# Kernel optimization log

Measured on AMD Instinct MI355X. Metric: run time of the kernel, lower is better.

Reference implementation:

```python
import jax, jax.numpy as jnp
import numpy as np

V = 128            # target_size (blank = V-1)
H = 2              # context_history_size
EMB = 128          # context_embedding_dim
ENC = 512          # enc_dim
PRED = 256         # pred_dim
JOIN = 512         # joiner_dim
B, T, U = 8, 512, 64


def setup_inputs() -> dict:
    key = jax.random.key(0)
    ks = jax.random.split(key, 12)
    s = lambda *d: 1.0 / np.sqrt(d[0])
    emb = jax.random.normal(ks[0], (V, EMB), jnp.float32) * 0.02
    emb = emb.at[V - 1].set(0.0)  # padding_idx row is zero
    inp = {
        "encoder_states": jax.random.normal(ks[1], (B, T, ENC), jnp.float32),
        "encoder_states_size": jnp.maximum(jax.random.randint(ks[2], (B,), 0, T + 1), 1).astype(jnp.int32),
        "targets": jax.random.randint(ks[3], (B, U), 0, V - 1, jnp.int64),
        "targets_size": jnp.maximum(jax.random.randint(ks[4], (B,), 0, U + 1), 1).astype(jnp.int32),
        "emb": emb,
        "W1": jax.random.normal(ks[5], (H * EMB, PRED), jnp.float32) * s(H * EMB),
        "b1": jnp.zeros((PRED,), jnp.float32),
        "W2": jax.random.normal(ks[6], (PRED, PRED), jnp.float32) * s(PRED),
        "b2": jnp.zeros((PRED,), jnp.float32),
        "Wj1": jax.random.normal(ks[7], (ENC + PRED, JOIN), jnp.float32) * s(ENC + PRED),
        "bj1": jnp.zeros((JOIN,), jnp.float32),
        "Wj2": jax.random.normal(ks[8], (JOIN, V), jnp.float32) * s(JOIN),
        "bj2": jnp.zeros((V,), jnp.float32),
    }
    return inp


def reference(encoder_states, encoder_states_size, targets, targets_size,
              emb, W1, b1, W2, b2, Wj1, bj1, Wj2, bj2):
    # ---- prediction network ----
    ext = jnp.pad(targets, ((0, 0), (H, 0)), constant_values=V - 1)  # [B, U+H]
    L = ext.shape[1]
    # context[..., i] = ext[:, H-1-i : L-i]  -> shape [B, U+1, H]
    context = jnp.stack([ext[:, H - 1 - i: L - i] for i in range(H)], axis=-1)
    e = emb[context].reshape(targets.shape[0], U + 1, H * EMB)  # [B, U+1, H*EMB]
    p = jax.nn.relu(e @ W1 + b1)
    pred = jax.nn.relu(p @ W2 + b2)                              # [B, U+1, PRED]

    # ---- joint network (dense masked T x (U+1) grid; concat-linear split into two GEMMs) ----
    We, Wp = Wj1[:ENC], Wj1[ENC:]
    enc_proj = jnp.einsum('bte,ej->btj', encoder_states, We)     # [B, T, JOIN]
    pred_proj = jnp.einsum('bup,pj->buj', pred, Wp)              # [B, U+1, JOIN]
    h = jax.nn.relu(enc_proj[:, :, None, :] + pred_proj[:, None, :, :] + bj1)  # [B,T,U+1,JOIN]
    logits = h @ Wj2 + bj2                                       # [B, T, U+1, V]

    t_idx = jnp.arange(T)[None, :, None]
    u_idx = jnp.arange(U + 1)[None, None, :]
    mask = (t_idx < encoder_states_size[:, None, None]) & (u_idx <= targets_size[:, None, None])
    return logits * mask[..., None].astype(logits.dtype)
```

## Files before the change

### kernel.cpp

```cpp
#include <hip/hip_runtime.h>


#define VOCAB 128
#define EMBD  128
#define ENCD  512
#define PREDD 256
#define JOIND 512
#define NB    8
#define NT    512
#define NUT   64
#define UP1   65
#define PRROWS 4

typedef __fp16   pk16x2 __attribute__((ext_vector_type(2)));
typedef _Float16 f16x8  __attribute__((ext_vector_type(8)));
typedef float    f32x4  __attribute__((ext_vector_type(4)));

__device__ __forceinline__ float frelu(float x) { return x > 0.f ? x : 0.f; }

__device__ __forceinline__ void splitf16_2(float x0, float x1,
                                           unsigned& hi, unsigned& lo) {
    pk16x2 h = __builtin_amdgcn_cvt_pkrtz(x0, x1);
    float r0 = x0 - (float)h.x;
    float r1 = x1 - (float)h.y;
    pk16x2 l = __builtin_amdgcn_cvt_pkrtz(r0, r1);
    __builtin_memcpy(&hi, &h, 4);
    __builtin_memcpy(&lo, &l, 4);
}

__global__ __launch_bounds__(256) void prep_weights(
    const float* __restrict__ Wj2, const float* __restrict__ Wj1,
    unsigned short* __restrict__ WjF, unsigned short* __restrict__ WeF)
{
    const int idx = blockIdx.x * 256 + threadIdx.x;
    float x; unsigned short* dst;
    if (idx < VOCAB * JOIND) {
        const int c = idx >> 12, rem = idx & 4095;
        const int n = rem >> 5, p = (rem >> 3) & 3, e = rem & 7;
        const int k = c * 32 + ((p ^ (n & 3)) << 3) + e;
        x = Wj2[k * VOCAB + n];
        dst = WjF + idx;
    } else {
        const int j = idx - VOCAB * JOIND;
        const int ct = j >> 16, rem1 = j & 65535;
        const int c = rem1 >> 12, rem = rem1 & 4095;
        const int nl = rem >> 5, p = (rem >> 3) & 3, e = rem & 7;
        const int n = ct * 128 + nl;
        const int k = c * 32 + ((p ^ (nl & 3)) << 3) + e;
        x = Wj1[(size_t)k * JOIND + n];
        dst = WeF + j;
    }
    const _Float16 h = (_Float16)x;
    unsigned short bits; __builtin_memcpy(&bits, &h, 2);
    *dst = bits;
}

__global__ __launch_bounds__(256, 3) void fused_pe(
    const int* __restrict__ targets, const int* __restrict__ tsz,
    const float* __restrict__ emb,
    const float* __restrict__ W1, const float* __restrict__ b1,
    const float* __restrict__ W2, const float* __restrict__ b2,
    const float* __restrict__ Wj1, const float* __restrict__ bj1,
    float* __restrict__ pproj,
    const float* __restrict__ A,
    const unsigned short* __restrict__ WeF,
    const int* __restrict__ esz, float* __restrict__ eproj)
{
    __shared__ __align__(16) unsigned char smem[24576];
    const int tid = threadIdx.x;

    if (blockIdx.x < 130) {
        float (*eS)[256] = (float(*)[256])smem;
        float (*pS)[256] = (float(*)[256])(smem + 4096);
        const int r0 = blockIdx.x * PRROWS;

        bool anyLive = false;
        #pragma unroll
        for (int i = 0; i < PRROWS; ++i) {
            const int row = r0 + i, b = row / UP1, u = row % UP1;
            anyLive = anyLive || (u <= tsz[b]);
        }
        if (!anyLive) return;

        #pragma unroll
        for (int i = 0; i < PRROWS; ++i) {
            const int row = r0 + i, b = row / UP1, u = row % UP1;
            const int c0 = (u >= 1) ? targets[b * NUT + u - 1] : (VOCAB - 1);
            const int c1 = (u >= 2) ? targets[b * NUT + u - 2] : (VOCAB - 1);
            eS[i][tid] = (tid < EMBD) ? emb[c0 * EMBD + tid]
                                      : emb[c1 * EMBD + (tid - EMBD)];
        }
        __syncthreads();
        {
            float f[PRROWS] = {};
            for (int k = 0; k < 256; k += 4) {
                const float w0 = W1[(k + 0) * PREDD + tid];
                const float w1 = W1[(k + 1) * PREDD + tid];
                const float w2 = W1[(k + 2) * PREDD + tid];
                const float w3 = W1[(k + 3) * PREDD + tid];
                #pragma unroll
                for (int i = 0; i < PRROWS; ++i) {
                    const float4 e = *(const float4*)&eS[i][k];
                    f[i] = fmaf(e.x, w0, fmaf(e.y, w1, fmaf(e.z, w2, fmaf(e.w, w3, f[i]))));
                }
            }
            const float bb = b1[tid];
            #pragma unroll
            for (int i = 0; i < PRROWS; ++i) pS[i][tid] = frelu(f[i] + bb);
        }
        __syncthreads();
        {
            float f[PRROWS] = {};
            for (int k = 0; k < 256; k += 4) {
                const float w0 = W2[(k + 0) * PREDD + tid];
                const float w1 = W2[(k + 1) * PREDD + tid];
                const float w2 = W2[(k + 2) * PREDD + tid];
                const float w3 = W2[(k + 3) * PREDD + tid];
                #pragma unroll
                for (int i = 0; i < PRROWS; ++i) {
                    const float4 p = *(const float4*)&pS[i][k];
                    f[i] = fmaf(p.x, w0, fmaf(p.y, w1, fmaf(p.z, w2, fmaf(p.w, w3, f[i]))));
                }
            }
            const float bb = b2[tid];
            #pragma unroll
            for (int i = 0; i < PRROWS; ++i) eS[i][tid] = frelu(f[i] + bb);
        }
        __syncthreads();
        #pragma unroll
        for (int h = 0; h < 2; ++h) {
            const int col = tid + h * 256;
            float g[PRROWS] = {};
            for (int k = 0; k < 256; k += 4) {
                const float w0 = Wj1[(size_t)(ENCD + k + 0) * JOIND + col];
                const float w1 = Wj1[(size_t)(ENCD + k + 1) * JOIND + col];
                const float w2 = Wj1[(size_t)(ENCD + k + 2) * JOIND + col];
                const float w3 = Wj1[(size_t)(ENCD + k + 3) * JOIND + col];
                #pragma unroll
                for (int i = 0; i < PRROWS; ++i) {
                    const float4 qv = *(const float4*)&eS[i][k];
                    g[i] = fmaf(qv.x, w0, fmaf(qv.y, w1, fmaf(qv.z, w2, fmaf(qv.w, w3, g[i]))));
                }
            }
            const float bb = bj1[col];
            #pragma unroll
            for (int i = 0; i < PRROWS; ++i)
                pproj[(size_t)(r0 + i) * JOIND + col] = g[i] + bb;
        }
        return;
    }

    unsigned short* AhS = (unsigned short*)smem;
    unsigned short* AlS = (unsigned short*)(smem + 8192);
    unsigned short* BhS = (unsigned short*)(smem + 16384);

    const int bxe = blockIdx.x - 130;
    const int rTile = bxe >> 2;
    const int ct = bxe & 3;
    const int b = rTile >> 2;
    const int t0 = (rTile & 3) * 128;
    if (t0 >= esz[b]) return;

    const int q = tid & 7;
    const float* ap[4]; int offA[4];
    #pragma unroll
    for (int p = 0; p < 4; ++p) {
        const int r = p * 32 + (tid >> 3);
        ap[p] = A + (size_t)(rTile * 128 + r) * ENCD + q * 4;
        offA[p] = r * 32 + (((q >> 1) ^ (r & 3)) << 3) + ((q & 1) << 2);
    }
    const size_t wbase = (size_t)ct * 65536;

    const int lane = tid & 63, w = tid >> 6;
    const int wr = w >> 1, wc = w & 1;
    const int l15 = lane & 15, lj = lane >> 4;
    const int sw = lj ^ (l15 & 3);

    f32x4 acc[4][4];
    #pragma unroll
    for (int mt = 0; mt < 4; ++mt)
        #pragma unroll
        for (int nt = 0; nt < 4; ++nt)
            acc[mt][nt] = (f32x4){0.f, 0.f, 0.f, 0.f};

    float4 aReg[4]; uint4 bReg0, bReg1;
    {
        #pragma unroll
        for (int p = 0; p < 4; ++p) aReg[p] = *(const float4*)(ap[p]);
        bReg0 = *(const uint4*)&WeF[wbase + (size_t)tid * 8];
        bReg1 = *(const uint4*)&WeF[wbase + (size_t)(tid + 256) * 8];
    }

    for (int c = 0; c < 16; ++c) {
        __syncthreads();
        #pragma unroll
        for (int p = 0; p < 4; ++p) {
            unsigned h0, h1, l0, l1;
            splitf16_2(aReg[p].x, aReg[p].y, h0, l0);
            splitf16_2(aReg[p].z, aReg[p].w, h1, l1);
            *(uint2*)&AhS[offA[p]] = make_uint2(h0, h1);
            *(uint2*)&AlS[offA[p]] = make_uint2(l0, l1);
        }
        *(uint4*)&BhS[tid * 8] = bReg0;
        *(uint4*)&BhS[(tid + 256) * 8] = bReg1;
        __syncthreads();
        if (c < 15) {
            const int kc = (c + 1) * 32;
            #pragma unroll
            for (int p = 0; p < 4; ++p) aReg[p] = *(const float4*)(ap[p] + kc);
            const size_t g = wbase + ((size_t)(c + 1) << 12);
            bReg0 = *(const uint4*)&WeF[g + (size_t)tid * 8];
            bReg1 = *(const uint4*)&WeF[g + (size_t)(tid + 256) * 8];
        }
        f16x8 bh[4];
        #pragma unroll
        for (int nt = 0; nt < 4; ++nt) {
            const int n = wc * 64 + nt * 16 + l15;
            bh[nt] = *(const f16x8*)&BhS[n * 32 + (sw << 3)];
        }
        #pragma unroll
        for (int mt = 0; mt < 4; ++mt) {
            const int m = wr * 64 + mt * 16 + l15;
            const int off = m * 32 + (sw << 3);
            const f16x8 ah = *(const f16x8*)&AhS[off];
            const f16x8 al = *(const f16x8*)&AlS[off];
            #pragma unroll
            for (int nt = 0; nt < 4; ++nt) {
                acc[mt][nt] = __builtin_amdgcn_mfma_f32_16x16x32_f16(ah, bh[nt], acc[mt][nt], 0, 0, 0);
                acc[mt][nt] = __builtin_amdgcn_mfma_f32_16x16x32_f16(al, bh[nt], acc[mt][nt], 0, 0, 0);
            }
        }
    }
    #pragma unroll
    for (int mt = 0; mt < 4; ++mt)
        #pragma unroll
        for (int r4 = 0; r4 < 4; ++r4) {
            const int row = wr * 64 + mt * 16 + lj * 4 + r4;
            float* dst = eproj + (size_t)(rTile * 128 + row) * JOIND
                       + ct * 128 + wc * 64 + l15;
            #pragma unroll
            for (int nt = 0; nt < 4; ++nt) dst[nt * 16] = acc[mt][nt][r4];
        }
}

__global__ __launch_bounds__(256, 3) void joint_kernel(
    const float* __restrict__ Eproj, const float* __restrict__ Pproj,
    const unsigned short* __restrict__ WjF,
    const float* __restrict__ bj2,
    const int* __restrict__ esz, const int* __restrict__ tsz,
    float* __restrict__ out)
{
    const int flat = blockIdx.x;
    const int logical = (flat & 7) * 288 + (flat >> 3);
    const int b  = logical / 288;
    const int rem = logical - b * 288;
    const int t0 = (rem / 9) * 16;
    const int u0 = (rem % 9) * 8;
    const int tid = threadIdx.x;
    const int es = esz[b], ts = tsz[b];
    const int nu = (UP1 - u0 < 8) ? (UP1 - u0) : 8;

    if (t0 >= es || u0 > ts) {
        const float4 z = {0.f, 0.f, 0.f, 0.f};
        const int total = 16 * nu * 32;
        for (int idx = tid; idx < total; idx += 256) {
            const int slot = idx & 31;
            const int rr = idx >> 5;
            const int tt = (nu == 8) ? (rr >> 3) : rr;
            const int uu = (nu == 8) ? (rr & 7) : 0;
            *(float4*)&out[(((size_t)(b * NT + t0 + tt) * UP1 + (u0 + uu)) << 7) + slot * 4] = z;
        }
        return;
    }

    __shared__ __align__(16) unsigned short BhS[128 * 32];
    __shared__ __align__(16) float eS[16 * 32];
    __shared__ __align__(16) float pS[8 * 32];

    const int erow = tid >> 3, es8 = tid & 7;
    const float* egp = Eproj + ((size_t)(b * NT + t0 + (erow & 15))) * JOIND + es8 * 4;
    float* elp = eS + (erow & 15) * 32 + ((es8 ^ (erow & 7)) << 2);
    const int prow = (tid >> 3) & 7, ps8 = tid & 7;
    int pu = u0 + prow; if (pu > NUT) pu = NUT;
    const float* pgp = Pproj + ((size_t)(b * UP1 + pu)) * JOIND + ps8 * 4;
    float* plp = pS + prow * 32 + ((ps8 ^ (prow & 7)) << 2);

    const int lane = tid & 63, w = tid >> 6;
    const int wr = w >> 1, wc = w & 1;
    const int l15 = lane & 15, lj = lane >> 4;
    const int sw = lj ^ (l15 & 3);
    const int urow = l15 & 7;
    const int po = urow * 32 + (((lj << 1) ^ (urow & 7)) << 2);
    int eo[4];
    #pragma unroll
    for (int mt = 0; mt < 4; ++mt) {
        const int trow = wr * 8 + mt * 2 + (l15 >> 3);
        eo[mt] = trow * 32 + (((lj << 1) ^ (trow & 7)) << 2);
    }
    int bo[4];
    #pragma unroll
    for (int nt = 0; nt < 4; ++nt)
        bo[nt] = (wc * 64 + nt * 16 + l15) * 32 + (sw << 3);

    f32x4 acc[4][4];
    #pragma unroll
    for (int mt = 0; mt < 4; ++mt)
        #pragma unroll
        for (int nt = 0; nt < 4; ++nt)
            acc[mt][nt] = (f32x4){0.f, 0.f, 0.f, 0.f};

    float4 aReg; uint4 bReg0, bReg1;
    {
        if (tid < 128)       aReg = *(const float4*)egp;
        else if (tid < 192)  aReg = *(const float4*)pgp;
        bReg0 = *(const uint4*)&WjF[(size_t)tid * 8];
        bReg1 = *(const uint4*)&WjF[(size_t)(tid + 256) * 8];
    }

    for (int c = 0; c < 16; ++c) {
        __syncthreads();
        if (tid < 128)      *(float4*)elp = aReg;
        else if (tid < 192) *(float4*)plp = aReg;
        *(uint4*)&BhS[tid * 8] = bReg0;
        *(uint4*)&BhS[(tid + 256) * 8] = bReg1;
        __syncthreads();
        if (c < 15) {
            const int kc = (c + 1) * 32;
            if (tid < 128)      aReg = *(const float4*)(egp + kc);
            else if (tid < 192) aReg = *(const float4*)(pgp + kc);
            const size_t g = (size_t)(c + 1) << 12;
            bReg0 = *(const uint4*)&WjF[g + (size_t)tid * 8];
            bReg1 = *(const uint4*)&WjF[g + (size_t)(tid + 256) * 8];
        }
        f16x8 bh[4];
        #pragma unroll
        for (int nt = 0; nt < 4; ++nt)
            bh[nt] = *(const f16x8*)&BhS[bo[nt]];
        const float4 pf0 = *(const float4*)&pS[po];
        const float4 pf1 = *(const float4*)&pS[po ^ 4];
        #pragma unroll
        for (int mt = 0; mt < 4; ++mt) {
            const float4 ef0 = *(const float4*)&eS[eo[mt]];
            const float4 ef1 = *(const float4*)&eS[eo[mt] ^ 4];
            const float x0 = frelu(ef0.x + pf0.x), x1 = frelu(ef0.y + pf0.y);
            const float x2 = frelu(ef0.z + pf0.z), x3 = frelu(ef0.w + pf0.w);
            const float x4 = frelu(ef1.x + pf1.x), x5 = frelu(ef1.y + pf1.y);
            const float x6 = frelu(ef1.z + pf1.z), x7 = frelu(ef1.w + pf1.w);
            unsigned h0, h1, h2, h3, l0, l1, l2, l3;
            splitf16_2(x0, x1, h0, l0); splitf16_2(x2, x3, h1, l1);
            splitf16_2(x4, x5, h2, l2); splitf16_2(x6, x7, h3, l3);
            uint4 ahv = make_uint4(h0, h1, h2, h3);
            uint4 alv = make_uint4(l0, l1, l2, l3);
            const f16x8 ah = *(const f16x8*)&ahv;
            const f16x8 al = *(const f16x8*)&alv;
            #pragma unroll
            for (int nt = 0; nt < 4; ++nt) {
                acc[mt][nt] = __builtin_amdgcn_mfma_f32_16x16x32_f16(ah, bh[nt], acc[mt][nt], 0, 0, 0);
                acc[mt][nt] = __builtin_amdgcn_mfma_f32_16x16x32_f16(al, bh[nt], acc[mt][nt], 0, 0, 0);
            }
        }
    }

    float bj[4];
    #pragma unroll
    for (int nt = 0; nt < 4; ++nt) bj[nt] = bj2[wc * 64 + nt * 16 + l15];

    #pragma unroll
    for (int mt = 0; mt < 4; ++mt) {
        #pragma unroll
        for (int r4 = 0; r4 < 4; ++r4) {
            const int row = wr * 64 + mt * 16 + lj * 4 + r4;
            const int t = t0 + (row >> 3);
            const int u = u0 + (row & 7);
            if (u >= UP1) continue;
            const bool valid = (t < es) && (u <= ts);
            float* __restrict__ orow =
                out + ((size_t)(b * NT + t) * UP1 + u) * VOCAB + wc * 64 + l15;
            #pragma unroll
            for (int nt = 0; nt < 4; ++nt)
                orow[nt * 16] = valid ? (acc[mt][nt][r4] + bj[nt]) : 0.f;
        }
    }
}

extern "C" void kernel_launch(void* const* d_in, const int* in_sizes, int n_in,
                              void* d_out, int out_size, void* d_ws, size_t ws_size,
                              hipStream_t stream) {
    (void)in_sizes; (void)n_in; (void)out_size; (void)ws_size;
    const float* enc     = (const float*)d_in[0];
    const int*   esz     = (const int*)d_in[1];
    const int*   targets = (const int*)d_in[2];
    const int*   tsz     = (const int*)d_in[3];
    const float* emb     = (const float*)d_in[4];
    const float* W1      = (const float*)d_in[5];
    const float* b1      = (const float*)d_in[6];
    const float* W2      = (const float*)d_in[7];
    const float* b2      = (const float*)d_in[8];
    const float* Wj1     = (const float*)d_in[9];
    const float* bj1     = (const float*)d_in[10];
    const float* Wj2     = (const float*)d_in[11];
    const float* bj2     = (const float*)d_in[12];
    float* out = (float*)d_out;

    float* eproj = (float*)d_ws;
    float* pproj = eproj + (size_t)NB * NT * JOIND;
    unsigned short* WjF = (unsigned short*)(pproj + (size_t)NB * UP1 * JOIND);
    unsigned short* WeF = WjF + 65536;

    prep_weights<<<1280, 256, 0, stream>>>(Wj2, Wj1, WjF, WeF);
    fused_pe<<<258, 256, 0, stream>>>(targets, tsz, emb, W1, b1, W2, b2,
                                      Wj1, bj1, pproj,
                                      enc, WeF, esz, eproj);
    joint_kernel<<<2304, 256, 0, stream>>>(eproj, pproj, WjF,
                                           bj2, esz, tsz, out);
}
```

Measured before the change: 232.6 us.

## Double-buffer LDS tiles in GEMM loops and register-block prediction MLP

The enc-proj GEMM and the joint kernel now keep two LDS buffers. Each iteration computes on the current buffer while the prefetched next chunk is stored into the other, which cuts one barrier per K-step. The prediction branch handles 8 rows per block with 4 rows × 2–4 columns per thread and register-prefetched weights, so fewer blocks are launched and each weight load is reused more. The cost is double the LDS footprint (48KB for fused_pe, larger for joint), which may lower occupancy.

After: 248.2 us. 6.7% more time.

```diff
diff --git a/kernel.cpp b/kernel.cpp
--- a/kernel.cpp
+++ b/kernel.cpp
@@ -10,7 +10,6 @@
 #define NT    512
 #define NUT   64
 #define UP1   65
-#define PRROWS 4
 
 typedef __fp16   pk16x2 __attribute__((ext_vector_type(2)));
 typedef _Float16 f16x8  __attribute__((ext_vector_type(8)));
@@ -55,6 +54,50 @@
     *dst = bits;
 }
 
+__device__ __forceinline__ void pred_layer(
+    const float (*in)[256], const float* __restrict__ W,
+    const float* __restrict__ bias, float (*out)[256], int rg, int c2)
+{
+    float f[4][2] = {};
+    float2 w[8], wn[8];
+    #pragma unroll
+    for (int j = 0; j < 8; ++j) w[j] = *(const float2*)&W[j * PREDD + c2];
+    for (int kb = 0; kb < 32; ++kb) {
+        const int k = kb * 8;
+        if (kb < 31) {
+            #pragma unroll
+            for (int j = 0; j < 8; ++j)
+                wn[j] = *(const float2*)&W[(k + 8 + j) * PREDD + c2];
+        }
+        #pragma unroll
+        for (int half = 0; half < 2; ++half) {
+            f32x4 iv[4];
+            #pragma unroll
+            for (int r = 0; r < 4; ++r)
+                iv[r] = *(const f32x4*)&in[rg + r][k + half * 4];
+            #pragma unroll
+            for (int jj = 0; jj < 4; ++jj) {
+                const int j = half * 4 + jj;
+                #pragma unroll
+                for (int r = 0; r < 4; ++r) {
+                    f[r][0] = fmaf(iv[r][jj], w[j].x, f[r][0]);
+                    f[r][1] = fmaf(iv[r][jj], w[j].y, f[r][1]);
+                }
+            }
+        }
+        if (kb < 31) {
+            #pragma unroll
+            for (int j = 0; j < 8; ++j) w[j] = wn[j];
+        }
+    }
+    const float2 bb = *(const float2*)&bias[c2];
+    #pragma unroll
+    for (int r = 0; r < 4; ++r) {
+        float2 o = {frelu(f[r][0] + bb.x), frelu(f[r][1] + bb.y)};
+        *(float2*)&out[rg + r][c2] = o;
+    }
+}
+
 __global__ __launch_bounds__(256, 3) void fused_pe(
     const int* __restrict__ targets, const int* __restrict__ tsz,
     const float* __restrict__ emb,
@@ -66,95 +109,91 @@
     const unsigned short* __restrict__ WeF,
     const int* __restrict__ esz, float* __restrict__ eproj)
 {
-    __shared__ __align__(16) unsigned char smem[24576];
+    __shared__ __align__(16) unsigned char smem[49152];
     const int tid = threadIdx.x;
 
-    if (blockIdx.x < 130) {
+    if (blockIdx.x < 65) {
         float (*eS)[256] = (float(*)[256])smem;
-        float (*pS)[256] = (float(*)[256])(smem + 4096);
-        const int r0 = blockIdx.x * PRROWS;
+        float (*pS)[256] = (float(*)[256])(smem + 8192);
+        const int r0 = blockIdx.x * 8;
 
         bool anyLive = false;
         #pragma unroll
-        for (int i = 0; i < PRROWS; ++i) {
-            const int row = r0 + i, b = row / UP1, u = row % UP1;
+        for (int i = 0; i < 8; ++i) {
+            const int row = r0 + i, b = row / UP1, u = row - b * UP1;
             anyLive = anyLive || (u <= tsz[b]);
         }
         if (!anyLive) return;
 
         #pragma unroll
-        for (int i = 0; i < PRROWS; ++i) {
-            const int row = r0 + i, b = row / UP1, u = row % UP1;
+        for (int i = 0; i < 8; ++i) {
+            const int row = r0 + i, b = row / UP1, u = row - b * UP1;
             const int c0 = (u >= 1) ? targets[b * NUT + u - 1] : (VOCAB - 1);
             const int c1 = (u >= 2) ? targets[b * NUT + u - 2] : (VOCAB - 1);
             eS[i][tid] = (tid < EMBD) ? emb[c0 * EMBD + tid]
                                       : emb[c1 * EMBD + (tid - EMBD)];
         }
         __syncthreads();
-        {
-            float f[PRROWS] = {};
-            for (int k = 0; k < 256; k += 4) {
-                const float w0 = W1[(k + 0) * PREDD + tid];
-                const float w1 = W1[(k + 1) * PREDD + tid];
-                const float w2 = W1[(k + 2) * PREDD + tid];
-                const float w3 = W1[(k + 3) * PREDD + tid];
+
+        const int wv = tid >> 6, lane = tid & 63;
+        const int rg = (wv & 1) * 4;
+        const int c2 = (wv >> 1) * 128 + lane * 2;
+
+        pred_layer(eS, W1, b1, pS, rg, c2);
+        __syncthreads();
+        pred_layer(pS, W2, b2, eS, rg, c2);
+        __syncthreads();
+
+        const int c4 = (wv >> 1) * 256 + lane * 4;
+        float g[4][4] = {};
+        f32x4 w4[8], wn4[8];
+        #pragma unroll
+        for (int j = 0; j < 8; ++j)
+            w4[j] = *(const f32x4*)&Wj1[(size_t)(ENCD + j) * JOIND + c4];
+        for (int kb = 0; kb < 32; ++kb) {
+            const int k = kb * 8;
+            if (kb < 31) {
                 #pragma unroll
-                for (int i = 0; i < PRROWS; ++i) {
-                    const float4 e = *(const float4*)&eS[i][k];
-                    f[i] = fmaf(e.x, w0, fmaf(e.y, w1, fmaf(e.z, w2, fmaf(e.w, w3, f[i]))));
+                for (int j = 0; j < 8; ++j)
+                    wn4[j] = *(const f32x4*)&Wj1[(size_t)(ENCD + k + 8 + j) * JOIND + c4];
+            }
+            #pragma unroll
+            for (int half = 0; half < 2; ++half) {
+                f32x4 iv[4];
+                #pragma unroll
+                for (int r = 0; r < 4; ++r)
+                    iv[r] = *(const f32x4*)&eS[rg + r][k + half * 4];
+                #pragma unroll
+                for (int jj = 0; jj < 4; ++jj) {
+                    const int j = half * 4 + jj;
+                    #pragma unroll
+                    for (int r = 0; r < 4; ++r)
+                        #pragma unroll
+                        for (int cc = 0; cc < 4; ++cc)
+                            g[r][cc] = fmaf(iv[r][jj], w4[j][cc], g[r][cc]);
                 }
             }
-            const float bb = b1[tid];
-            #pragma unroll
-            for (int i = 0; i < PRROWS; ++i) pS[i][tid] = frelu(f[i] + bb);
-        }
-        __syncthreads();
-        {
-            float f[PRROWS] = {};
-            for (int k = 0; k < 256; k += 4) {
-                const float w0 = W2[(k + 0) * PREDD + tid];
-                const float w1 = W2[(k + 1) * PREDD + tid];
-                const float w2 = W2[(k + 2) * PREDD + tid];
-                const float w3 = W2[(k + 3) * PREDD + tid];
+            if (kb < 31) {
                 #pragma unroll
-                for (int i = 0; i < PRROWS; ++i) {
-                    const float4 p = *(const float4*)&pS[i][k];
-                    f[i] = fmaf(p.x, w0, fmaf(p.y, w1, fmaf(p.z, w2, fmaf(p.w, w3, f[i]))));
-                }
-            }
-            const float bb = b2[tid];
-            #pragma unroll
-            for (int i = 0; i < PRROWS; ++i) eS[i][tid] = frelu(f[i] + bb);
-        }
-        __syncthreads();
-        #pragma unroll
-        for (int h = 0; h < 2; ++h) {
-            const int col = tid + h * 256;
-            float g[PRROWS] = {};
-            for (int k = 0; k < 256; k += 4) {
-                const float w0 = Wj1[(size_t)(ENCD + k + 0) * JOIND + col];
-                const float w1 = Wj1[(size_t)(ENCD + k + 1) * JOIND + col];
-                const float w2 = Wj1[(size_t)(ENCD + k + 2) * JOIND + col];
-                const float w3 = Wj1[(size_t)(ENCD + k + 3) * JOIND + col];
-                #pragma unroll
-                for (int i = 0; i < PRROWS; ++i) {
-                    const float4 qv = *(const float4*)&eS[i][k];
-                    g[i] = fmaf(qv.x, w0, fmaf(qv.y, w1, fmaf(qv.z, w2, fmaf(qv.w, w3, g[i]))));
-                }
-            }
-            const float bb = bj1[col];
-            #pragma unroll
-            for (int i = 0; i < PRROWS; ++i)
-                pproj[(size_t)(r0 + i) * JOIND + col] = g[i] + bb;
+                for (int j = 0; j < 8; ++j) w4[j] = wn4[j];
+            }
+        }
+        const f32x4 bb4 = *(const f32x4*)&bj1[c4];
+        #pragma unroll
+        for (int r = 0; r < 4; ++r) {
+            f32x4 o;
+            #pragma unroll
+            for (int cc = 0; cc < 4; ++cc) o[cc] = g[r][cc] + bb4[cc];
+            *(f32x4*)&pproj[(size_t)(r0 + rg + r) * JOIND + c4] = o;
         }
         return;
     }
 
-    unsigned short* AhS = (unsigned short*)smem;
-    unsigned short* AlS = (unsigned short*)(smem + 8192);
-    unsigned short* BhS = (unsigned short*)(smem + 16384);
-
-    const int bxe = blockIdx.x - 130;
+    unsigned short (*AhS)[4096] = (unsigned short(*)[4096])smem;
+    unsigned short (*AlS)[4096] = (unsigned short(*)[4096])(smem + 16384);
+    unsigned short (*BhS)[4096] = (unsigned short(*)[4096])(smem + 32768);
+
+    const int bxe = blockIdx.x - 65;
     const int rTile = bxe >> 2;
     const int ct = bxe & 3;
     const int b = rTile >> 2;
@@ -184,26 +223,24 @@
             acc[mt][nt] = (f32x4){0.f, 0.f, 0.f, 0.f};
 
     float4 aReg[4]; uint4 bReg0, bReg1;
-    {
-        #pragma unroll
-        for (int p = 0; p < 4; ++p) aReg[p] = *(const float4*)(ap[p]);
-        bReg0 = *(const uint4*)&WeF[wbase + (size_t)tid * 8];
-        bReg1 = *(const uint4*)&WeF[wbase + (size_t)(tid + 256) * 8];
-    }
+    #pragma unroll
+    for (int p = 0; p < 4; ++p) aReg[p] = *(const float4*)(ap[p]);
+    bReg0 = *(const uint4*)&WeF[wbase + (size_t)tid * 8];
+    bReg1 = *(const uint4*)&WeF[wbase + (size_t)(tid + 256) * 8];
+    #pragma unroll
+    for (int p = 0; p < 4; ++p) {
+        unsigned h0, h1, l0, l1;
+        splitf16_2(aReg[p].x, aReg[p].y, h0, l0);
+        splitf16_2(aReg[p].z, aReg[p].w, h1, l1);
+        *(uint2*)&AhS[0][offA[p]] = make_uint2(h0, h1);
+        *(uint2*)&AlS[0][offA[p]] = make_uint2(l0, l1);
+    }
+    *(uint4*)&BhS[0][tid * 8] = bReg0;
+    *(uint4*)&BhS[0][(tid + 256) * 8] = bReg1;
+    __syncthreads();
 
     for (int c = 0; c < 16; ++c) {
-        __syncthreads();
-        #pragma unroll
-        for (int p = 0; p < 4; ++p) {
-            unsigned h0, h1, l0, l1;
-            splitf16_2(aReg[p].x, aReg[p].y, h0, l0);
-            splitf16_2(aReg[p].z, aReg[p].w, h1, l1);
-            *(uint2*)&AhS[offA[p]] = make_uint2(h0, h1);
-            *(uint2*)&AlS[offA[p]] = make_uint2(l0, l1);
-        }
-        *(uint4*)&BhS[tid * 8] = bReg0;
-        *(uint4*)&BhS[(tid + 256) * 8] = bReg1;
-        __syncthreads();
+        const int cur = c & 1, nxt = cur ^ 1;
         if (c < 15) {
             const int kc = (c + 1) * 32;
             #pragma unroll
@@ -216,20 +253,33 @@
         #pragma unroll
         for (int nt = 0; nt < 4; ++nt) {
             const int n = wc * 64 + nt * 16 + l15;
-            bh[nt] = *(const f16x8*)&BhS[n * 32 + (sw << 3)];
+            bh[nt] = *(const f16x8*)&BhS[cur][n * 32 + (sw << 3)];
         }
         #pragma unroll
         for (int mt = 0; mt < 4; ++mt) {
             const int m = wr * 64 + mt * 16 + l15;
             const int off = m * 32 + (sw << 3);
-            const f16x8 ah = *(const f16x8*)&AhS[off];
-            const f16x8 al = *(const f16x8*)&AlS[off];
+            const f16x8 ah = *(const f16x8*)&AhS[cur][off];
+            const f16x8 al = *(const f16x8*)&AlS[cur][off];
             #pragma unroll
             for (int nt = 0; nt < 4; ++nt) {
                 acc[mt][nt] = __builtin_amdgcn_mfma_f32_16x16x32_f16(ah, bh[nt], acc[mt][nt], 0, 0, 0);
                 acc[mt][nt] = __builtin_amdgcn_mfma_f32_16x16x32_f16(al, bh[nt], acc[mt][nt], 0, 0, 0);
             }
         }
+        if (c < 15) {
+            #pragma unroll
+            for (int p = 0; p < 4; ++p) {
+                unsigned h0, h1, l0, l1;
+                splitf16_2(aReg[p].x, aReg[p].y, h0, l0);
+                splitf16_2(aReg[p].z, aReg[p].w, h1, l1);
+                *(uint2*)&AhS[nxt][offA[p]] = make_uint2(h0, h1);
+                *(uint2*)&AlS[nxt][offA[p]] = make_uint2(l0, l1);
+            }
+            *(uint4*)&BhS[nxt][tid * 8] = bReg0;
+            *(uint4*)&BhS[nxt][(tid + 256) * 8] = bReg1;
+        }
+        __syncthreads();
     }
     #pragma unroll
     for (int mt = 0; mt < 4; ++mt)
@@ -273,17 +323,17 @@
         return;
     }
 
-    __shared__ __align__(16) unsigned short BhS[128 * 32];
-    __shared__ __align__(16) float eS[16 * 32];
-    __shared__ __align__(16) float pS[8 * 32];
+    __shared__ __align__(16) unsigned short BhS[2][128 * 32];
+    __shared__ __align__(16) float eS[2][16 * 32];
+    __shared__ __align__(16) float pS[2][8 * 32];
 
     const int erow = tid >> 3, es8 = tid & 7;
     const float* egp = Eproj + ((size_t)(b * NT + t0 + (erow & 15))) * JOIND + es8 * 4;
-    float* elp = eS + (erow & 15) * 32 + ((es8 ^ (erow & 7)) << 2);
+    const int elpo = (erow & 15) * 32 + ((es8 ^ (erow & 7)) << 2);
     const int prow = (tid >> 3) & 7, ps8 = tid & 7;
     int pu = u0 + prow; if (pu > NUT) pu = NUT;
     const float* pgp = Pproj + ((size_t)(b * UP1 + pu)) * JOIND + ps8 * 4;
-    float* plp = pS + prow * 32 + ((ps8 ^ (prow & 7)) << 2);
+    const int plpo = prow * 32 + ((ps8 ^ (prow & 7)) << 2);
 
     const int lane = tid & 63, w = tid >> 6;
     const int wr = w >> 1, wc = w & 1;
@@ -310,20 +360,18 @@
             acc[mt][nt] = (f32x4){0.f, 0.f, 0.f, 0.f};
 
     float4 aReg; uint4 bReg0, bReg1;
-    {
-        if (tid < 128)       aReg = *(const float4*)egp;
-        else if (tid < 192)  aReg = *(const float4*)pgp;
-        bReg0 = *(const uint4*)&WjF[(size_t)tid * 8];
-        bReg1 = *(const uint4*)&WjF[(size_t)(tid + 256) * 8];
-    }
+    if (tid < 128)       aReg = *(const float4*)egp;
+    else if (tid < 192)  aReg = *(const float4*)pgp;
+    bReg0 = *(const uint4*)&WjF[(size_t)tid * 8];
+    bReg1 = *(const uint4*)&WjF[(size_t)(tid + 256) * 8];
+    if (tid < 128)      *(float4*)&eS[0][elpo] = aReg;
+    else if (tid < 192) *(float4*)&pS[0][plpo] = aReg;
+    *(uint4*)&BhS[0][tid * 8] = bReg0;
+    *(uint4*)&BhS[0][(tid + 256) * 8] = bReg1;
+    __syncthreads();
 
     for (int c = 0; c < 16; ++c) {
-        __syncthreads();
-        if (tid < 128)      *(float4*)elp = aReg;
-        else if (tid < 192) *(float4*)plp = aReg;
-        *(uint4*)&BhS[tid * 8] = bReg0;
-        *(uint4*)&BhS[(tid + 256) * 8] = bReg1;
-        __syncthreads();
+        const int cur = c & 1, nxt = cur ^ 1;
         if (c < 15) {
             const int kc = (c + 1) * 32;
             if (tid < 128)      aReg = *(const float4*)(egp + kc);
@@ -335,13 +383,13 @@
         f16x8 bh[4];
         #pragma unroll
         for (int nt = 0; nt < 4; ++nt)
-            bh[nt] = *(const f16x8*)&BhS[bo[nt]];
-        const float4 pf0 = *(const float4*)&pS[po];
-        const float4 pf1 = *(const float4*)&pS[po ^ 4];
+            bh[nt] = *(const f16x8*)&BhS[cur][bo[nt]];
+        const float4 pf0 = *(const float4*)&pS[cur][po];
+        const float4 pf1 = *(const float4*)&pS[cur][po ^ 4];
         #pragma unroll
         for (int mt = 0; mt < 4; ++mt) {
-            const float4 ef0 = *(const float4*)&eS[eo[mt]];
-            const float4 ef1 = *(const float4*)&eS[eo[mt] ^ 4];
+            const float4 ef0 = *(const float4*)&eS[cur][eo[mt]];
+            const float4 ef1 = *(const float4*)&eS[cur][eo[mt] ^ 4];
             const float x0 = frelu(ef0.x + pf0.x), x1 = frelu(ef0.y + pf0.y);
             const float x2 = frelu(ef0.z + pf0.z), x3 = frelu(ef0.w + pf0.w);
             const float x4 = frelu(ef1.x + pf1.x), x5 = frelu(ef1.y + pf1.y);
@@ -359,6 +407,13 @@
                 acc[mt][nt] = __builtin_amdgcn_mfma_f32_16x16x32_f16(al, bh[nt], acc[mt][nt], 0, 0, 0);
             }
         }
+        if (c < 15) {
+            if (tid < 128)      *(float4*)&eS[nxt][elpo] = aReg;
+            else if (tid < 192) *(float4*)&pS[nxt][plpo] = aReg;
+            *(uint4*)&BhS[nxt][tid * 8] = bReg0;
+            *(uint4*)&BhS[nxt][(tid + 256) * 8] = bReg1;
+        }
+        __syncthreads();
     }
 
     float bj[4];
@@ -408,7 +463,7 @@
     unsigned short* WeF = WjF + 65536;
 
     prep_weights<<<1280, 256, 0, stream>>>(Wj2, Wj1, WjF, WeF);
-    fused_pe<<<258, 256, 0, stream>>>(targets, tsz, emb, W1, b1, W2, b2,
+    fused_pe<<<193, 256, 0, stream>>>(targets, tsz, emb, W1, b1, W2, b2,
                                       Wj1, bj1, pproj,
                                       enc, WeF, esz, eproj);
     joint_kernel<<<2304, 256, 0, stream>>>(eproj, pproj, WjF,
```
